# Performance work log

Hardware: AMD Instinct MI355X
Metric: run time of the kernel (lower is better)

Reference implementation:

```python
import jax, jax.numpy as jnp
import numpy as np

N = 50000       # nodes
E = 800000      # edges (before self-loops)
F = 128         # input features
H = 4           # heads
C = 64          # hidden per head
NC = 40         # classes
NEG_SLOPE = 0.2  # PyG GATConv default leaky relu slope


def _glorot(key, shape):
    fan = sum(shape[-2:]) if len(shape) >= 2 else shape[-1] * 2
    return jax.random.normal(key, shape, jnp.float32) * jnp.sqrt(2.0 / fan)


def gat_conv(x, W, a_src, a_dst, bias, src, dst, concat):
    """PyG-style GATConv (eval mode, self-loops already in src/dst).
    x:[N,Fin] W:[Fin,H*C] a_src,a_dst:[H,C] bias:[H*C] or [C]."""
    n = x.shape[0]
    h_, c_ = a_src.shape
    h = (x @ W).reshape(n, h_, c_)                      # [N,H,C]
    al_s = jnp.einsum('nhc,hc->nh', h, a_src)           # [N,H]
    al_d = jnp.einsum('nhc,hc->nh', h, a_dst)
    logits = jax.nn.leaky_relu(al_s[src] + al_d[dst], NEG_SLOPE)  # [E,H]
    # segment softmax over incoming edges of each dst node
    mx = jax.ops.segment_max(logits, dst, num_segments=n)
    mx = jnp.where(jnp.isfinite(mx), mx, 0.0)
    ex = jnp.exp(logits - mx[dst])
    den = jax.ops.segment_sum(ex, dst, num_segments=n)
    alpha = ex / (den[dst] + 1e-16)                     # [E,H]
    msg = h[src] * alpha[:, :, None]                    # [E,H,C]
    out = jax.ops.segment_sum(msg, dst, num_segments=n) # [N,H,C]
    if concat:
        return out.reshape(n, h_ * c_) + bias
    return out.mean(axis=1) + bias


def setup_inputs() -> dict:
    key = jax.random.key(0)
    ks = jax.random.split(key, 16)
    x = jax.random.normal(ks[0], (N, F), jnp.float32)
    edge_index = jax.random.randint(ks[1], (2, E), 0, N, jnp.int64)
    HC = H * C
    return {
        'x': x, 'edge_index': edge_index,
        'W1': _glorot(ks[2], (F, HC)),   'a1_src': _glorot(ks[3], (H, C)),
        'a1_dst': _glorot(ks[4], (H, C)), 'b1': jnp.zeros((HC,), jnp.float32),
        'W2': _glorot(ks[5], (HC, HC)),  'a2_src': _glorot(ks[6], (H, C)),
        'a2_dst': _glorot(ks[7], (H, C)), 'b2': jnp.zeros((HC,), jnp.float32),
        'W3': _glorot(ks[8], (HC, H * NC)), 'a3_src': _glorot(ks[9], (H, NC)),
        'a3_dst': _glorot(ks[10], (H, NC)), 'b3': jnp.zeros((NC,), jnp.float32),
    }


def reference(x, edge_index, W1, a1_src, a1_dst, b1, W2, a2_src, a2_dst, b2,
              W3, a3_src, a3_dst, b3):
    n = x.shape[0]
    loop = jnp.arange(n, dtype=edge_index.dtype)
    src = jnp.concatenate([edge_index[0], loop])
    dst = jnp.concatenate([edge_index[1], loop])
    x1 = jax.nn.elu(gat_conv(x, W1, a1_src, a1_dst, b1, src, dst, True))
    x2 = jax.nn.elu(gat_conv(x1, W2, a2_src, a2_dst, b2, src, dst, True) + x1)
    out = gat_conv(x2, W3, a3_src, a3_dst, b3, src, dst, False)  # [N,NC]
    return out
```

## Files before the change

### kernel.cpp

```cpp
#include <hip/hip_runtime.h>
#include <hip/hip_bf16.h>
#include <hip/hip_fp16.h>
#include <math.h>

#define NEG_SLOPE 0.2f

typedef _Float16 half8 __attribute__((ext_vector_type(8)));
typedef _Float16 half4 __attribute__((ext_vector_type(4)));
typedef float f32x4 __attribute__((ext_vector_type(4)));

__global__ void degree_kernel(const int* __restrict__ ei, int E, int n,
                              int* __restrict__ deg) {
    int e = blockIdx.x * 256 + threadIdx.x;
    int tot = E + n;
    if (e >= tot) return;
    int d = (e < E) ? ei[E + e] : (e - E);
    atomicAdd(&deg[d], 1);
}

__global__ __launch_bounds__(1024) void scan_block(const int* __restrict__ deg,
                                                   int* __restrict__ row_off,
                                                   int* __restrict__ bsums, int n) {
    __shared__ int tmp[1024];
    int t = threadIdx.x;
    int idx = blockIdx.x * 1024 + t;
    int v = (idx < n) ? deg[idx] : 0;
    tmp[t] = v;
    __syncthreads();
    #pragma unroll
    for (int off = 1; off < 1024; off <<= 1) {
        int x = (t >= off) ? tmp[t - off] : 0;
        __syncthreads();
        tmp[t] += x;
        __syncthreads();
    }
    if (idx < n) row_off[idx] = tmp[t] - v;
    if (t == 1023) bsums[blockIdx.x] = tmp[1023];
}

__global__ __launch_bounds__(64) void scan_sums(int* __restrict__ bsums, int nb,
                                                int* __restrict__ row_off, int n) {
    int lane = threadIdx.x;
    int carry = 0;
    for (int base = 0; base < nb; base += 64) {
        int i = base + lane;
        int o = (i < nb) ? bsums[i] : 0;
        int v = o;
        #pragma unroll
        for (int off = 1; off < 64; off <<= 1) {
            int x = __shfl_up(v, off, 64);
            if (lane >= off) v += x;
        }
        if (i < nb) bsums[i] = carry + v - o;
        int tot = __shfl(v, 63, 64);
        carry += tot;
    }
    if (lane == 0) row_off[n] = carry;
}

__global__ __launch_bounds__(1024) void scan_add(int* __restrict__ row_off,
                                                 const int* __restrict__ bsums,
                                                 int* __restrict__ cursor, int n) {
    int idx = blockIdx.x * 1024 + threadIdx.x;
    if (idx < n) {
        int v = row_off[idx] + bsums[blockIdx.x];
        row_off[idx] = v;
        cursor[idx] = v;
    }
}

__global__ void scatter_kernel(const int* __restrict__ ei, int E, int n,
                               int* __restrict__ cursor, int* __restrict__ csr_src) {
    int e = blockIdx.x * 256 + threadIdx.x;
    int tot = E + n;
    if (e >= tot) return;
    int s, d;
    if (e < E) { s = ei[e]; d = ei[E + e]; } else { s = d = e - E; }
    int pos = atomicAdd(&cursor[d], 1);
    csr_src[pos] = s;
}

__global__ void split_f32x4(const float* __restrict__ src, _Float16* __restrict__ hi,
                            _Float16* __restrict__ lo, int n4) {
    int i = blockIdx.x * 256 + threadIdx.x;
    if (i >= n4) return;
    float4 v = ((const float4*)src)[i];
    half4 h, l;
    h.x = (_Float16)v.x; l.x = (_Float16)(v.x - (float)h.x);
    h.y = (_Float16)v.y; l.y = (_Float16)(v.y - (float)h.y);
    h.z = (_Float16)v.z; l.z = (_Float16)(v.z - (float)h.z);
    h.w = (_Float16)v.w; l.w = (_Float16)(v.w - (float)h.w);
    ((half4*)hi)[i] = h;
    ((half4*)lo)[i] = l;
}

__global__ void wt_split_all(const float* __restrict__ W1, const float* __restrict__ W2,
                             const float* __restrict__ W3,
                             _Float16* __restrict__ b1h, _Float16* __restrict__ b1l,
                             _Float16* __restrict__ b2h, _Float16* __restrict__ b2l,
                             _Float16* __restrict__ b3h, _Float16* __restrict__ b3l) {
    int idx = blockIdx.x * 256 + threadIdx.x;
    const float* W; _Float16 *bh, *bl; int K, N, li;
    if (idx < 256 * 128) {
        W = W1; bh = b1h; bl = b1l; K = 128; N = 256; li = idx;
    } else if (idx < 256 * 128 + 256 * 256) {
        W = W2; bh = b2h; bl = b2l; K = 256; N = 256; li = idx - 256 * 128;
    } else if (idx < 256 * 128 + 2 * 256 * 256) {
        W = W3; bh = b3h; bl = b3l; K = 256; N = 160; li = idx - 256 * 128 - 256 * 256;
    } else return;
    int n = li / K, k = li % K;
    float v = (n < N) ? W[(size_t)k * N + n] : 0.f;
    _Float16 h = (_Float16)v;
    bh[li] = h;
    bl[li] = (_Float16)(v - (float)h);
}

template <int NK, bool FUSE>
__global__ __launch_bounds__(256, 1) void gemm_mfma(const _Float16* __restrict__ Ahi,
                                                    const _Float16* __restrict__ Alo,
                                                    const _Float16* __restrict__ Bthi,
                                                    const _Float16* __restrict__ Btlo,
                                                    _Float16* __restrict__ Ch,
                                                    const float* __restrict__ a_src,
                                                    const float* __restrict__ a_dst,
                                                    float* __restrict__ als,
                                                    float* __restrict__ ald,
                                                    int M, int N) {
    constexpr int K = NK * 32;
    __shared__ _Float16 Ah[2][2][64 * 32];
    int t = threadIdx.x;
    int wave = t >> 6, lane = t & 63;
    int row0 = blockIdx.x * 64;

    auto lds_off = [](int m, int g0) -> int {
        int P = m >> 1;
        int gp = ((m & 1) << 2) | g0;
        return P * 64 + ((gp ^ (P & 7)) << 3);
    };

    int r0 = t >> 2, g0 = t & 3;
    int off0 = lds_off(r0, g0);
    bool mok = (row0 + r0) < M;
    const _Float16* aph = Ahi + (size_t)(row0 + r0) * K + g0 * 8;
    const _Float16* apl = Alo + (size_t)(row0 + r0) * K + g0 * 8;

    half8 svh, svl;
    auto stage_load = [&](int k0) {
        svh = svl = (half8)(_Float16)0.f;
        if (mok) { svh = *(const half8*)(aph + k0); svl = *(const half8*)(apl + k0); }
    };
    auto stage_write = [&](int buf) {
        *(half8*)(&Ah[buf][0][off0]) = svh;
        *(half8*)(&Ah[buf][1][off0]) = svl;
    };

    const _Float16* bhp[4];
    const _Float16* blp[4];
    #pragma unroll
    for (int nf = 0; nf < 4; nf++) {
        int n = wave * 64 + nf * 16 + (lane & 15);
        bhp[nf] = Bthi + (size_t)n * K + (lane >> 4) * 8;
        blp[nf] = Btlo + (size_t)n * K + (lane >> 4) * 8;
    }

    f32x4 acc[4][4];
    #pragma unroll
    for (int i = 0; i < 4; i++)
        #pragma unroll
        for (int j = 0; j < 4; j++)
            acc[i][j] = (f32x4)0.f;

    stage_load(0);
    stage_write(0);
    half8 bh[4], bl[4];
    #pragma unroll
    for (int nf = 0; nf < 4; nf++) {
        bh[nf] = *(const half8*)(bhp[nf]);
        bl[nf] = *(const half8*)(blp[nf]);
    }
    __syncthreads();

    #pragma unroll
    for (int kt = 0; kt < NK; kt++) {
        int cur = kt & 1;
        half8 bh2[4], bl2[4];
        if (kt + 1 < NK) {
            stage_load((kt + 1) * 32);
            #pragma unroll
            for (int nf = 0; nf < 4; nf++) {
                bh2[nf] = *(const half8*)(bhp[nf] + (kt + 1) * 32);
                bl2[nf] = *(const half8*)(blp[nf] + (kt + 1) * 32);
            }
        }
        half8 ah[4], al[4];
        #pragma unroll
        for (int mf = 0; mf < 4; mf++) {
            int m = mf * 16 + (lane & 15);
            int off = lds_off(m, lane >> 4);
            ah[mf] = *(half8*)(&Ah[cur][0][off]);
            al[mf] = *(half8*)(&Ah[cur][1][off]);
        }
        #pragma unroll
        for (int mf = 0; mf < 4; mf++)
            #pragma unroll
            for (int nf = 0; nf < 4; nf++) {
                acc[mf][nf] = __builtin_amdgcn_mfma_f32_16x16x32_f16(
                    ah[mf], bh[nf], acc[mf][nf], 0, 0, 0);
                acc[mf][nf] = __builtin_amdgcn_mfma_f32_16x16x32_f16(
                    ah[mf], bl[nf], acc[mf][nf], 0, 0, 0);
                acc[mf][nf] = __builtin_amdgcn_mfma_f32_16x16x32_f16(
                    al[mf], bh[nf], acc[mf][nf], 0, 0, 0);
            }
        if (kt + 1 < NK) {
            stage_write(cur ^ 1);
            __syncthreads();
            #pragma unroll
            for (int nf = 0; nf < 4; nf++) { bh[nf] = bh2[nf]; bl[nf] = bl2[nf]; }
        }
    }

    #pragma unroll
    for (int mf = 0; mf < 4; mf++)
        #pragma unroll
        for (int nf = 0; nf < 4; nf++) {
            int col = wave * 64 + nf * 16 + (lane & 15);
            if (col >= N) continue;
            #pragma unroll
            for (int q = 0; q < 4; q++) {
                int row = row0 + mf * 16 + (lane >> 4) * 4 + q;
                if (row < M)
                    Ch[(size_t)row * N + col] = (_Float16)acc[mf][nf][q];
            }
        }

    if (FUSE) {
        float asv[4], adv[4];
        #pragma unroll
        for (int nf = 0; nf < 4; nf++) {
            int cih = nf * 16 + (lane & 15);
            asv[nf] = a_src[wave * 64 + cih];
            adv[nf] = a_dst[wave * 64 + cih];
        }
        #pragma unroll
        for (int mf = 0; mf < 4; mf++)
            #pragma unroll
            for (int q = 0; q < 4; q++) {
                float ss = 0.f, sd = 0.f;
                #pragma unroll
                for (int nf = 0; nf < 4; nf++) {
                    float v = acc[mf][nf][q];
                    ss = fmaf(v, asv[nf], ss);
                    sd = fmaf(v, adv[nf], sd);
                }
                #pragma unroll
                for (int off = 8; off >= 1; off >>= 1) {
                    ss += __shfl_xor(ss, off, 64);
                    sd += __shfl_xor(sd, off, 64);
                }
                int row = row0 + mf * 16 + (lane >> 4) * 4 + q;
                if ((lane & 15) == 0 && row < M) {
                    als[row * 4 + wave] = ss;
                    ald[row * 4 + wave] = sd;
                }
            }
    }
}

template <int C>
__global__ __launch_bounds__(256) void coef_kernel(const _Float16* __restrict__ h,
                                                   const float* __restrict__ a_src,
                                                   const float* __restrict__ a_dst,
                                                   float* __restrict__ als,
                                                   float* __restrict__ ald, int n) {
    int wave = threadIdx.x >> 6;
    int lane = threadIdx.x & 63;
    int node = blockIdx.x * 4 + wave;
    if (node >= n) return;
    const _Float16* hr = h + (size_t)node * (4 * C);
    float ps[4], pd[4];
    #pragma unroll
    for (int hh = 0; hh < 4; hh++) {
        float hv = (lane < C) ? (float)hr[hh * C + lane] : 0.f;
        float as_ = (lane < C) ? a_src[hh * C + lane] : 0.f;
        float ad_ = (lane < C) ? a_dst[hh * C + lane] : 0.f;
        ps[hh] = hv * as_;
        pd[hh] = hv * ad_;
    }
    #pragma unroll
    for (int off = 32; off >= 1; off >>= 1) {
        #pragma unroll
        for (int hh = 0; hh < 4; hh++) {
            ps[hh] += __shfl_xor(ps[hh], off, 64);
            pd[hh] += __shfl_xor(pd[hh], off, 64);
        }
    }
    if (lane == 0) {
        #pragma unroll
        for (int hh = 0; hh < 4; hh++) {
            als[node * 4 + hh] = ps[hh];
            ald[node * 4 + hh] = pd[hh];
        }
    }
}

template <int C, int MODE>
__global__ __launch_bounds__(256) void agg_kernel(const __half* __restrict__ hhp,
                                                  const float* __restrict__ als,
                                                  const float* __restrict__ ald,
                                                  const int* __restrict__ row_off,
                                                  const int* __restrict__ csr_src,
                                                  const float* __restrict__ bias,
                                                  const _Float16* __restrict__ rh,
                                                  const _Float16* __restrict__ rl,
                                                  float* __restrict__ outf,
                                                  _Float16* __restrict__ oh,
                                                  _Float16* __restrict__ ol, int n) {
    constexpr int HC = 4 * C;
    constexpr int LPN = HC / 8;
    constexpr int LPH = C / 8;
    const _Float16* hh = (const _Float16*)hhp;

    int t = threadIdx.x;
    int wave = t >> 6, lane = t & 63;
    int l = lane & 31;
    int node = (blockIdx.x * 4 + wave) * 2 + (lane >> 5);
    bool nact = node < n;
    bool lact = nact && (l < LPN);
    int g = (l < LPN) ? (l / LPH) : 0;

    int rs = 0, cnt = 0;
    if (lact) {
        rs = row_off[node];
        cnt = row_off[node + 1] - rs;
    }
    float aldg = lact ? ald[node * 4 + g] : 0.f;

    float acc[8] = {};
    float den = 0.f;

    if (cnt > 0) {
        int sA[8];
        float avA[8];
        #pragma unroll
        for (int q = 0; q < 8; q++) {
            int idx = q < cnt ? q : cnt - 1;
            sA[q] = csr_src[rs + idx];
        }
        #pragma unroll
        for (int q = 0; q < 8; q++) avA[q] = als[sA[q] * 4 + g];

        for (int base = 0; base < cnt; base += 8) {
            half8 hv[8];
            #pragma unroll
            for (int q = 0; q < 8; q++)
                hv[q] = *(const half8*)(hh + (size_t)sA[q] * HC + l * 8);

            int sB[8];
            float avB[8];
            if (base + 8 < cnt) {
                #pragma unroll
                for (int q = 0; q < 8; q++) {
                    int idx = base + 8 + q; if (idx >= cnt) idx = cnt - 1;
                    sB[q] = csr_src[rs + idx];
                }
                #pragma unroll
                for (int q = 0; q < 8; q++) avB[q] = als[sB[q] * 4 + g];
            }

            float ex[8];
            #pragma unroll
            for (int q = 0; q < 8; q++) {
                float lg = avA[q] + aldg;
                lg = (lg > 0.f) ? lg : NEG_SLOPE * lg;
                float e = __expf(lg);
                ex[q] = (base + q < cnt) ? e : 0.f;
                den += ex[q];
            }
            #pragma unroll
            for (int q = 0; q < 8; q++) {
                #pragma unroll
                for (int k = 0; k < 8; k++)
                    acc[k] = fmaf(ex[q], (float)hv[q][k], acc[k]);
            }
            #pragma unroll
            for (int q = 0; q < 8; q++) { sA[q] = sB[q]; avA[q] = avB[q]; }
        }
    }

    float inv = 1.f / (den + 1e-16f);
    float v[8];
    #pragma unroll
    for (int k = 0; k < 8; k++) v[k] = acc[k] * inv;

    if (MODE == 2) {
        float vs[8];
        #pragma unroll
        for (int k = 0; k < 8; k++) vs[k] = v[k];
        #pragma unroll
        for (int k2 = 1; k2 < 4; k2++) {
            #pragma unroll
            for (int k = 0; k < 8; k++)
                vs[k] += __shfl(v[k], lane + 5 * k2, 64);
        }
        if (nact && l < 5) {
            float b[8];
            *(float4*)&b[0] = *(const float4*)(bias + l * 8);
            *(float4*)&b[4] = *(const float4*)(bias + l * 8 + 4);
            float o[8];
            #pragma unroll
            for (int k = 0; k < 8; k++) o[k] = vs[k] * 0.25f + b[k];
            *(float4*)(outf + (size_t)node * C + l * 8)     = make_float4(o[0], o[1], o[2], o[3]);
            *(float4*)(outf + (size_t)node * C + l * 8 + 4) = make_float4(o[4], o[5], o[6], o[7]);
        }
    } else {
        if (lact) {
            float b[8];
            *(float4*)&b[0] = *(const float4*)(bias + l * 8);
            *(float4*)&b[4] = *(const float4*)(bias + l * 8 + 4);
            float o[8];
            #pragma unroll
            for (int k = 0; k < 8; k++) o[k] = v[k] + b[k];
            if (MODE == 1) {
                size_t ridx = (size_t)node * HC + l * 8;
                half8 r_h = *(const half8*)(rh + ridx);
                half8 r_l = *(const half8*)(rl + ridx);
                #pragma unroll
                for (int k = 0; k < 8; k++) o[k] += (float)r_h[k] + (float)r_l[k];
            }
            #pragma unroll
            for (int k = 0; k < 8; k++) o[k] = (o[k] > 0.f) ? o[k] : expm1f(o[k]);
            half8 hv8, lv8;
            #pragma unroll
            for (int k = 0; k < 8; k++) {
                hv8[k] = (_Float16)o[k];
                lv8[k] = (_Float16)(o[k] - (float)hv8[k]);
            }
            size_t oidx = (size_t)node * HC + l * 8;
            *(half8*)(oh + oidx) = hv8;
            *(half8*)(ol + oidx) = lv8;
        }
    }
}

extern "C" void kernel_launch(void* const* d_in, const int* in_sizes, int n_in,
                              void* d_out, int out_size, void* d_ws, size_t ws_size,
                              hipStream_t stream) {
    const float* x   = (const float*)d_in[0];
    const int*   ei  = (const int*)d_in[1];
    const float* W1  = (const float*)d_in[2];
    const float* a1s = (const float*)d_in[3];
    const float* a1d = (const float*)d_in[4];
    const float* b1  = (const float*)d_in[5];
    const float* W2  = (const float*)d_in[6];
    const float* a2s = (const float*)d_in[7];
    const float* a2d = (const float*)d_in[8];
    const float* b2  = (const float*)d_in[9];
    const float* W3  = (const float*)d_in[10];
    const float* a3s = (const float*)d_in[11];
    const float* a3d = (const float*)d_in[12];
    const float* b3  = (const float*)d_in[13];
    float* out = (float*)d_out;

    int N = in_sizes[0] / 128;
    int E = in_sizes[1] / 2;

    char* ws = (char*)d_ws;
    size_t off = 0;
    auto alloc = [&](size_t bytes) -> void* {
        void* p = ws + off;
        off += (bytes + 255) & ~(size_t)255;
        return p;
    };
    _Float16* hhalf = (_Float16*)alloc((size_t)N * 256 * 2);
    _Float16* pA_hi = (_Float16*)alloc((size_t)N * 256 * 2);
    _Float16* pA_lo = (_Float16*)alloc((size_t)N * 256 * 2);
    _Float16* pB_hi = (_Float16*)alloc((size_t)N * 256 * 2);
    _Float16* pB_lo = (_Float16*)alloc((size_t)N * 256 * 2);
    float*    als   = (float*)alloc((size_t)N * 4 * 4);
    float*    ald   = (float*)alloc((size_t)N * 4 * 4);
    _Float16* bt1h  = (_Float16*)alloc(256 * 128 * 2);
    _Float16* bt1l  = (_Float16*)alloc(256 * 128 * 2);
    _Float16* bt2h  = (_Float16*)alloc(256 * 256 * 2);
    _Float16* bt2l  = (_Float16*)alloc(256 * 256 * 2);
    _Float16* bt3h  = (_Float16*)alloc(256 * 256 * 2);
    _Float16* bt3l  = (_Float16*)alloc(256 * 256 * 2);
    int* deg     = (int*)alloc((size_t)N * 4);
    int* row_off = (int*)alloc((size_t)(N + 1) * 4);
    int* cursor  = (int*)alloc((size_t)N * 4);
    int* csr     = (int*)alloc((size_t)(E + N) * 4);
    int* bsums   = (int*)alloc(1024 * 4);

    int tot = E + N;
    int nb = (N + 1023) / 1024;
    hipMemsetAsync(deg, 0, (size_t)N * 4, stream);
    degree_kernel<<<(tot + 255) / 256, 256, 0, stream>>>(ei, E, N, deg);
    scan_block<<<nb, 1024, 0, stream>>>(deg, row_off, bsums, N);
    scan_sums<<<1, 64, 0, stream>>>(bsums, nb, row_off, N);
    scan_add<<<nb, 1024, 0, stream>>>(row_off, bsums, cursor, N);
    scatter_kernel<<<(tot + 255) / 256, 256, 0, stream>>>(ei, E, N, cursor, csr);

    {
        int n4 = N * 128 / 4;
        split_f32x4<<<(n4 + 255) / 256, 256, 0, stream>>>(x, pA_hi, pA_lo, n4);
        int wtot = 256 * 128 + 2 * 256 * 256;
        wt_split_all<<<(wtot + 255) / 256, 256, 0, stream>>>(W1, W2, W3,
            bt1h, bt1l, bt2h, bt2l, bt3h, bt3l);
    }

    int nodeBlocks4 = (N + 3) / 4;
    int pairs = (N + 1) / 2;
    int aggBlocks = (pairs + 3) / 4;
    dim3 blk(256);
    dim3 ggrid((N + 63) / 64);

    gemm_mfma<4, true><<<ggrid, blk, 0, stream>>>(pA_hi, pA_lo, bt1h, bt1l, hhalf,
                                                  a1s, a1d, als, ald, N, 256);
    agg_kernel<64, 0><<<aggBlocks, blk, 0, stream>>>((const __half*)hhalf, als, ald,
        row_off, csr, b1, nullptr, nullptr, nullptr, pB_hi, pB_lo, N);

    gemm_mfma<8, true><<<ggrid, blk, 0, stream>>>(pB_hi, pB_lo, bt2h, bt2l, hhalf,
                                                  a2s, a2d, als, ald, N, 256);
    agg_kernel<64, 1><<<aggBlocks, blk, 0, stream>>>((const __half*)hhalf, als, ald,
        row_off, csr, b2, pB_hi, pB_lo, nullptr, pA_hi, pA_lo, N);

    gemm_mfma<8, false><<<ggrid, blk, 0, stream>>>(pA_hi, pA_lo, bt3h, bt3l, hhalf,
                                                   nullptr, nullptr, nullptr, nullptr, N, 160);
    coef_kernel<40><<<nodeBlocks4, blk, 0, stream>>>(hhalf, a3s, a3d, als, ald, N);
    agg_kernel<40, 2><<<aggBlocks, blk, 0, stream>>>((const __half*)hhalf, als, ald,
        row_off, csr, b3, nullptr, nullptr, out, nullptr, nullptr, N);
}
```

Baseline: 459.6 us.

## Merge prep kernels into one launch and simplify GEMM B-fragment prefetch

The input split, weight split and degree-count kernels are merged into a single prep kernel whose blocks branch on block index, which removes two launches and lets the three independent jobs run side by side. In the MFMA GEMM, the register double-buffering of B fragments is replaced by loading them at the start of each k-step, and the launch bound drops the min-blocks hint of 1. The aim is lower register pressure and possibly higher occupancy, at the cost of exposing B-load latency inside each k-step.

```diff
diff --git a/kernel.cpp b/kernel.cpp
--- a/kernel.cpp
+++ b/kernel.cpp
@@ -9,13 +9,50 @@
 typedef _Float16 half4 __attribute__((ext_vector_type(4)));
 typedef float f32x4 __attribute__((ext_vector_type(4)));
 
-__global__ void degree_kernel(const int* __restrict__ ei, int E, int n,
-                              int* __restrict__ deg) {
-    int e = blockIdx.x * 256 + threadIdx.x;
-    int tot = E + n;
-    if (e >= tot) return;
-    int d = (e < E) ? ei[E + e] : (e - E);
-    atomicAdd(&deg[d], 1);
+__global__ __launch_bounds__(256) void prep_kernel(
+        const float* __restrict__ x, _Float16* __restrict__ xhi,
+        _Float16* __restrict__ xlo, int n4,
+        const float* __restrict__ W1, const float* __restrict__ W2,
+        const float* __restrict__ W3,
+        _Float16* __restrict__ b1h, _Float16* __restrict__ b1l,
+        _Float16* __restrict__ b2h, _Float16* __restrict__ b2l,
+        _Float16* __restrict__ b3h, _Float16* __restrict__ b3l,
+        const int* __restrict__ ei, int E, int n, int* __restrict__ deg,
+        int nbSplit, int nbWt) {
+    int b = blockIdx.x;
+    if (b < nbSplit) {
+        int i = b * 256 + threadIdx.x;
+        if (i >= n4) return;
+        float4 v = ((const float4*)x)[i];
+        half4 h, l;
+        h.x = (_Float16)v.x; l.x = (_Float16)(v.x - (float)h.x);
+        h.y = (_Float16)v.y; l.y = (_Float16)(v.y - (float)h.y);
+        h.z = (_Float16)v.z; l.z = (_Float16)(v.z - (float)h.z);
+        h.w = (_Float16)v.w; l.w = (_Float16)(v.w - (float)h.w);
+        ((half4*)xhi)[i] = h;
+        ((half4*)xlo)[i] = l;
+    } else if (b < nbSplit + nbWt) {
+        int idx = (b - nbSplit) * 256 + threadIdx.x;
+        const float* W; _Float16 *bh, *bl; int K, N, li;
+        if (idx < 256 * 128) {
+            W = W1; bh = b1h; bl = b1l; K = 128; N = 256; li = idx;
+        } else if (idx < 256 * 128 + 256 * 256) {
+            W = W2; bh = b2h; bl = b2l; K = 256; N = 256; li = idx - 256 * 128;
+        } else if (idx < 256 * 128 + 2 * 256 * 256) {
+            W = W3; bh = b3h; bl = b3l; K = 256; N = 160; li = idx - 256 * 128 - 256 * 256;
+        } else return;
+        int nn = li / K, k = li % K;
+        float v = (nn < N) ? W[(size_t)k * N + nn] : 0.f;
+        _Float16 h = (_Float16)v;
+        bh[li] = h;
+        bl[li] = (_Float16)(v - (float)h);
+    } else {
+        int e = (b - nbSplit - nbWt) * 256 + threadIdx.x;
+        int tot = E + n;
+        if (e >= tot) return;
+        int d = (e < E) ? ei[E + e] : (e - E);
+        atomicAdd(&deg[d], 1);
+    }
 }
 
 __global__ __launch_bounds__(1024) void scan_block(const int* __restrict__ deg,
@@ -80,52 +117,17 @@
     csr_src[pos] = s;
 }
 
-__global__ void split_f32x4(const float* __restrict__ src, _Float16* __restrict__ hi,
-                            _Float16* __restrict__ lo, int n4) {
-    int i = blockIdx.x * 256 + threadIdx.x;
-    if (i >= n4) return;
-    float4 v = ((const float4*)src)[i];
-    half4 h, l;
-    h.x = (_Float16)v.x; l.x = (_Float16)(v.x - (float)h.x);
-    h.y = (_Float16)v.y; l.y = (_Float16)(v.y - (float)h.y);
-    h.z = (_Float16)v.z; l.z = (_Float16)(v.z - (float)h.z);
-    h.w = (_Float16)v.w; l.w = (_Float16)(v.w - (float)h.w);
-    ((half4*)hi)[i] = h;
-    ((half4*)lo)[i] = l;
-}
-
-__global__ void wt_split_all(const float* __restrict__ W1, const float* __restrict__ W2,
-                             const float* __restrict__ W3,
-                             _Float16* __restrict__ b1h, _Float16* __restrict__ b1l,
-                             _Float16* __restrict__ b2h, _Float16* __restrict__ b2l,
-                             _Float16* __restrict__ b3h, _Float16* __restrict__ b3l) {
-    int idx = blockIdx.x * 256 + threadIdx.x;
-    const float* W; _Float16 *bh, *bl; int K, N, li;
-    if (idx < 256 * 128) {
-        W = W1; bh = b1h; bl = b1l; K = 128; N = 256; li = idx;
-    } else if (idx < 256 * 128 + 256 * 256) {
-        W = W2; bh = b2h; bl = b2l; K = 256; N = 256; li = idx - 256 * 128;
-    } else if (idx < 256 * 128 + 2 * 256 * 256) {
-        W = W3; bh = b3h; bl = b3l; K = 256; N = 160; li = idx - 256 * 128 - 256 * 256;
-    } else return;
-    int n = li / K, k = li % K;
-    float v = (n < N) ? W[(size_t)k * N + n] : 0.f;
-    _Float16 h = (_Float16)v;
-    bh[li] = h;
-    bl[li] = (_Float16)(v - (float)h);
-}
-
 template <int NK, bool FUSE>
-__global__ __launch_bounds__(256, 1) void gemm_mfma(const _Float16* __restrict__ Ahi,
-                                                    const _Float16* __restrict__ Alo,
-                                                    const _Float16* __restrict__ Bthi,
-                                                    const _Float16* __restrict__ Btlo,
-                                                    _Float16* __restrict__ Ch,
-                                                    const float* __restrict__ a_src,
-                                                    const float* __restrict__ a_dst,
-                                                    float* __restrict__ als,
-                                                    float* __restrict__ ald,
-                                                    int M, int N) {
+__global__ __launch_bounds__(256) void gemm_mfma(const _Float16* __restrict__ Ahi,
+                                                 const _Float16* __restrict__ Alo,
+                                                 const _Float16* __restrict__ Bthi,
+                                                 const _Float16* __restrict__ Btlo,
+                                                 _Float16* __restrict__ Ch,
+                                                 const float* __restrict__ a_src,
+                                                 const float* __restrict__ a_dst,
+                                                 float* __restrict__ als,
+                                                 float* __restrict__ ald,
+                                                 int M, int N) {
     constexpr int K = NK * 32;
     __shared__ _Float16 Ah[2][2][64 * 32];
     int t = threadIdx.x;
@@ -172,26 +174,20 @@
 
     stage_load(0);
     stage_write(0);
-    half8 bh[4], bl[4];
-    #pragma unroll
-    for (int nf = 0; nf < 4; nf++) {
-        bh[nf] = *(const half8*)(bhp[nf]);
-        bl[nf] = *(const half8*)(blp[nf]);
-    }
     __syncthreads();
 
     #pragma unroll
     for (int kt = 0; kt < NK; kt++) {
         int cur = kt & 1;
-        half8 bh2[4], bl2[4];
-        if (kt + 1 < NK) {
-            stage_load((kt + 1) * 32);
-            #pragma unroll
-            for (int nf = 0; nf < 4; nf++) {
-                bh2[nf] = *(const half8*)(bhp[nf] + (kt + 1) * 32);
-                bl2[nf] = *(const half8*)(blp[nf] + (kt + 1) * 32);
-            }
-        }
+        int k0 = kt * 32;
+        half8 bh[4], bl[4];
+        #pragma unroll
+        for (int nf = 0; nf < 4; nf++) {
+            bh[nf] = *(const half8*)(bhp[nf] + k0);
+            bl[nf] = *(const half8*)(blp[nf] + k0);
+        }
+        if (kt + 1 < NK) stage_load((kt + 1) * 32);
+
         half8 ah[4], al[4];
         #pragma unroll
         for (int mf = 0; mf < 4; mf++) {
@@ -214,8 +210,6 @@
         if (kt + 1 < NK) {
             stage_write(cur ^ 1);
             __syncthreads();
-            #pragma unroll
-            for (int nf = 0; nf < 4; nf++) { bh[nf] = bh2[nf]; bl[nf] = bl2[nf]; }
         }
     }
 
@@ -492,20 +486,21 @@
 
     int tot = E + N;
     int nb = (N + 1023) / 1024;
+    int n4 = N * 128 / 4;
+    int nbSplit = (n4 + 255) / 256;
+    int wtot = 256 * 128 + 2 * 256 * 256;
+    int nbWt = (wtot + 255) / 256;
+    int nbDeg = (tot + 255) / 256;
+
     hipMemsetAsync(deg, 0, (size_t)N * 4, stream);
-    degree_kernel<<<(tot + 255) / 256, 256, 0, stream>>>(ei, E, N, deg);
+    prep_kernel<<<nbSplit + nbWt + nbDeg, 256, 0, stream>>>(
+        x, pA_hi, pA_lo, n4, W1, W2, W3,
+        bt1h, bt1l, bt2h, bt2l, bt3h, bt3l,
+        ei, E, N, deg, nbSplit, nbWt);
     scan_block<<<nb, 1024, 0, stream>>>(deg, row_off, bsums, N);
     scan_sums<<<1, 64, 0, stream>>>(bsums, nb, row_off, N);
     scan_add<<<nb, 1024, 0, stream>>>(row_off, bsums, cursor, N);
     scatter_kernel<<<(tot + 255) / 256, 256, 0, stream>>>(ei, E, N, cursor, csr);
-
-    {
-        int n4 = N * 128 / 4;
-        split_f32x4<<<(n4 + 255) / 256, 256, 0, stream>>>(x, pA_hi, pA_lo, n4);
-        int wtot = 256 * 128 + 2 * 256 * 256;
-        wt_split_all<<<(wtot + 255) / 256, 256, 0, stream>>>(W1, W2, W3,
-            bt1h, bt1l, bt2h, bt2l, bt3h, bt3l);
-    }
 
     int nodeBlocks4 = (N + 3) / 4;
     int pairs = (N + 1) / 2;
```

Measured after the change: 450.7 us. Within noise of the previous version (-1.9%).
